# Optimization experiments

Measured on AMD Instinct MI355X. Metric: run time of the kernel, lower is better.

## Reference

```python
import jax, jax.numpy as jnp
import numpy as np

N = 100000          # nodes
E = 1600000         # edges (avg degree 16)
H = 128             # hidden_dim
P = 10              # INVARIANT_PHYSICS_DIM
TOTAL = P + H
LN_EPS = 1e-5       # torch LayerNorm default


def setup_inputs() -> dict:
    key = jax.random.key(0)
    ks = jax.random.split(key, 16)
    s = 0.02
    return {
        "physics_x": jax.random.normal(ks[0], (N, P), dtype=jnp.float32),
        "learnable_emb": jax.random.normal(ks[1], (N, H), dtype=jnp.float32),
        "edge_index": jax.random.randint(ks[2], (2, E), 0, N, dtype=jnp.int32),
        "Wq": jax.random.normal(ks[3], (TOTAL, H), dtype=jnp.float32) * s,
        "bq": jnp.zeros((H,), dtype=jnp.float32),
        "Wk": jax.random.normal(ks[4], (TOTAL, H), dtype=jnp.float32) * s,
        "bk": jnp.zeros((H,), dtype=jnp.float32),
        "Wv": jax.random.normal(ks[5], (H, H), dtype=jnp.float32) * s,
        "bv": jnp.zeros((H,), dtype=jnp.float32),
        "Wo": jax.random.normal(ks[6], (H, H), dtype=jnp.float32) * s,
        "bo": jnp.zeros((H,), dtype=jnp.float32),
        "gamma": jnp.ones((H,), dtype=jnp.float32),
        "beta": jnp.zeros((H,), dtype=jnp.float32),
    }


def reference(physics_x, learnable_emb, edge_index, Wq, bq, Wk, bk, Wv, bv, Wo, bo, gamma, beta):
    n_nodes = learnable_emb.shape[0]
    scale = 1.0 / np.sqrt(Wq.shape[1]).astype(np.float32)

    full_repr = jnp.concatenate([physics_x, learnable_emb], axis=-1)   # [N, P+H]
    Q = full_repr @ Wq + bq                                            # [N, H]
    K = full_repr @ Wk + bk                                            # [N, H]
    V = learnable_emb @ Wv + bv                                        # [N, H]

    src, dst = edge_index[0], edge_index[1]
    # per-edge unnormalized attention (NOTE: no max-subtraction, faithful to source)
    attn_scores = jnp.sum(Q[dst] * K[src], axis=-1) * scale            # [E]
    exp_scores = jnp.exp(attn_scores)                                  # [E]
    denom = jax.ops.segment_sum(exp_scores, dst, num_segments=n_nodes) # [N]
    attn_probs = exp_scores / (denom[dst] + 1e-8)                      # [E]

    msg = V[src] * attn_probs[:, None]                                 # [E, H]
    agg = jax.ops.segment_sum(msg, dst, num_segments=n_nodes)          # [N, H]

    out = agg @ Wo + bo
    x = learnable_emb + out
    mu = jnp.mean(x, axis=-1, keepdims=True)
    var = jnp.var(x, axis=-1, keepdims=True)
    return gamma * (x - mu) / jnp.sqrt(var + LN_EPS) + beta
```

## Files before the change

kernel.cpp:

```cpp
#include <hip/hip_runtime.h>
#include <hip/hip_bf16.h>
#include <math.h>

#define PDIM 10
#define HDIM 128
#define TDIM 138
#define AROW 168
#define B_LEN (5 * 8 * 64 * 8)
#define TROW 136

#define CW_WQ 0
#define CW_WK 17664
#define CW_WV 35328
#define CW_WO 51712
#define CW_BQ 68096
#define CW_BK 68224
#define CW_BV 68352
#define CW_BO 68480
#define CW_GA 68608
#define CW_BE 68736
#define CW_TOTAL 68864

typedef short v8s __attribute__((ext_vector_type(8)));
typedef float v4f __attribute__((ext_vector_type(4)));
typedef float v2f __attribute__((ext_vector_type(2)));

#if defined(__has_builtin)
#if __has_builtin(__builtin_amdgcn_cvt_pk_f32_fp8) && __has_builtin(__builtin_amdgcn_cvt_pk_fp8_f32)
#define HAVE_FP8_CVT 1
#endif
#endif
#ifndef HAVE_FP8_CVT
#define HAVE_FP8_CVT 0
#endif

__device__ __forceinline__ float b2f_lo(unsigned u) { return __uint_as_float(u << 16); }
__device__ __forceinline__ float b2f_hi(unsigned u) { return __uint_as_float(u & 0xffff0000u); }
__device__ __forceinline__ unsigned short f2b(float f) {
    unsigned u = __float_as_uint(f);
    u += 0x7fffu + ((u >> 16) & 1u);
    return (unsigned short)(u >> 16);
}

__device__ __forceinline__ float f8_dec1(unsigned b) {
    unsigned e = (b >> 3) & 0xf, m = b & 7;
    float v = e ? __uint_as_float(((e + 120) << 23) | (m << 20))
                : (float)m * 0.001953125f;
    return (b & 0x80) ? -v : v;
}
__device__ __forceinline__ unsigned f8_enc1(float f) {
    unsigned u = __float_as_uint(f);
    unsigned s = (u >> 31) << 7;
    float a = fabsf(f);
    if (a < 0.0009765625f) return s;
    if (a < 0.015625f) {
        int m = (int)(a * 512.f + 0.5f); if (m > 7) m = 7;
        return s | (unsigned)m;
    }
    if (a >= 448.f) return s | 0x7e;
    int ex = (int)((u >> 23) & 0xff);
    unsigned mant = u & 0x7fffff;
    unsigned r = mant >> 20, rem = mant & 0xfffff;
    if (rem > 0x80000u || (rem == 0x80000u && (r & 1))) r++;
    if (r == 8) { r = 0; ex++; }
    if (ex - 127 > 8) return s | 0x7e;
    return s | (unsigned)((ex - 120) << 3) | r;
}

__device__ __forceinline__ void dot4(unsigned w, const float* q, float& p) {
#if HAVE_FP8_CVT
    v2f lo = __builtin_amdgcn_cvt_pk_f32_fp8((int)w, false);
    v2f hi = __builtin_amdgcn_cvt_pk_f32_fp8((int)w, true);
    p = fmaf(q[0], lo[0], p); p = fmaf(q[1], lo[1], p);
    p = fmaf(q[2], hi[0], p); p = fmaf(q[3], hi[1], p);
#else
    p = fmaf(q[0], f8_dec1(w & 0xff), p);
    p = fmaf(q[1], f8_dec1((w >> 8) & 0xff), p);
    p = fmaf(q[2], f8_dec1((w >> 16) & 0xff), p);
    p = fmaf(q[3], f8_dec1(w >> 24), p);
#endif
}
__device__ __forceinline__ void acc4(unsigned w, float e, float* acc) {
#if HAVE_FP8_CVT
    v2f lo = __builtin_amdgcn_cvt_pk_f32_fp8((int)w, false);
    v2f hi = __builtin_amdgcn_cvt_pk_f32_fp8((int)w, true);
    acc[0] = fmaf(e, lo[0], acc[0]); acc[1] = fmaf(e, lo[1], acc[1]);
    acc[2] = fmaf(e, hi[0], acc[2]); acc[3] = fmaf(e, hi[1], acc[3]);
#else
    acc[0] = fmaf(e, f8_dec1(w & 0xff), acc[0]);
    acc[1] = fmaf(e, f8_dec1((w >> 8) & 0xff), acc[1]);
    acc[2] = fmaf(e, f8_dec1((w >> 16) & 0xff), acc[2]);
    acc[3] = fmaf(e, f8_dec1(w >> 24), acc[3]);
#endif
}
__device__ __forceinline__ uint2 pack8(uint4 t) {
#if HAVE_FP8_CVT
    int u0 = __builtin_amdgcn_cvt_pk_fp8_f32(b2f_lo(t.x), b2f_hi(t.x), 0, false);
    u0 = __builtin_amdgcn_cvt_pk_fp8_f32(b2f_lo(t.y), b2f_hi(t.y), u0, true);
    int u1 = __builtin_amdgcn_cvt_pk_fp8_f32(b2f_lo(t.z), b2f_hi(t.z), 0, false);
    u1 = __builtin_amdgcn_cvt_pk_fp8_f32(b2f_lo(t.w), b2f_hi(t.w), u1, true);
    return make_uint2((unsigned)u0, (unsigned)u1);
#else
    unsigned u0 = f8_enc1(b2f_lo(t.x)) | (f8_enc1(b2f_hi(t.x)) << 8)
                | (f8_enc1(b2f_lo(t.y)) << 16) | (f8_enc1(b2f_hi(t.y)) << 24);
    unsigned u1 = f8_enc1(b2f_lo(t.z)) | (f8_enc1(b2f_hi(t.z)) << 8)
                | (f8_enc1(b2f_lo(t.w)) << 16) | (f8_enc1(b2f_hi(t.w)) << 24);
    return make_uint2(u0, u1);
#endif
}

__global__ void ws_sentinel_kernel(float* out, int bucket)
{
    if (threadIdx.x == 0) out[0] = ldexpf(1.f + (float)bucket / 256.f, 100);
}

__global__ __launch_bounds__(256) void convert_weights(
    const float* Wq, const float* Wk, const float* Wv, const float* Wo,
    const float* bq, const float* bk, const float* bv, const float* bo,
    const float* ga, const float* be,
    float* __restrict__ dst)
{
    int idx = blockIdx.x * 256 + threadIdx.x;
    if (idx >= CW_TOTAL) return;
    const float* src; int loc;
    if      (idx < CW_WK) { src = Wq; loc = idx - CW_WQ; }
    else if (idx < CW_WV) { src = Wk; loc = idx - CW_WK; }
    else if (idx < CW_WO) { src = Wv; loc = idx - CW_WV; }
    else if (idx < CW_BQ) { src = Wo; loc = idx - CW_WO; }
    else if (idx < CW_BK) { src = bq; loc = idx - CW_BQ; }
    else if (idx < CW_BV) { src = bk; loc = idx - CW_BK; }
    else if (idx < CW_BO) { src = bv; loc = idx - CW_BV; }
    else if (idx < CW_GA) { src = bo; loc = idx - CW_BO; }
    else if (idx < CW_BE) { src = ga; loc = idx - CW_GA; }
    else                  { src = be; loc = idx - CW_BE; }
    dst[idx] = src[loc];
}

__global__ __launch_bounds__(256) void pack_wfrag(
    const float* __restrict__ cw, unsigned short* __restrict__ wfrag)
{
    int g = blockIdx.x * 256 + threadIdx.x;
    if (g >= 3 * 5 * 8 * 64) return;
    int lane = g & 63;
    int nt   = (g >> 6) & 7;
    int mk   = g >> 9;
    int kc = mk % 5, mat = mk / 5;
    int quad = lane >> 4, l15 = lane & 15;
    int n = nt * 16 + l15;

    unsigned short* dst = wfrag + (size_t)g * 8;
    #pragma unroll
    for (int j = 0; j < 8; ++j) {
        int k = kc * 32 + quad * 8 + j;
        float v = 0.f;
        if (mat == 0)      { if (k < TDIM) v = cw[CW_WQ + k * HDIM + n]; }
        else if (mat == 1) { if (k < TDIM) v = cw[CW_WK + k * HDIM + n]; }
        else               { if (k >= PDIM && k < TDIM) v = cw[CW_WV + (k - PDIM) * HDIM + n]; }
        dst[j] = f2b(v);
    }
}

__global__ __launch_bounds__(256, 5) void qkv_mfma_kernel(
    const float* __restrict__ physics, const float* __restrict__ emb,
    const float* __restrict__ cw, const unsigned short* __restrict__ wfrag,
    unsigned short* __restrict__ Qb, unsigned char* __restrict__ K8,
    unsigned char* __restrict__ V8, int n_nodes)
{
    __shared__ __align__(16) unsigned short smem[64 * AROW];

    const int tid = threadIdx.x;
    const int nbase = blockIdx.x * 64;
    const int lane = tid & 63;
    const int w = tid >> 6;
    const int quad = lane >> 4;
    const int l15 = lane & 15;

    for (int idx = tid; idx < 64 * 5; idx += 256) {
        int r = idx / 5, p = idx - r * 5;
        int node = nbase + r;
        float v0 = 0.f, v1 = 0.f;
        if (node < n_nodes) {
            const float* ph = physics + (size_t)node * PDIM + 2 * p;
            v0 = ph[0]; v1 = ph[1];
        }
        ((unsigned*)smem)[r * 84 + p] = (unsigned)f2b(v0) | ((unsigned)f2b(v1) << 16);
    }
    for (int idx = tid; idx < 64 * 32; idx += 256) {
        int r = idx >> 5, c = idx & 31;
        int node = nbase + r;
        float4 e = make_float4(0.f, 0.f, 0.f, 0.f);
        if (node < n_nodes) e = *(const float4*)(emb + (size_t)node * HDIM + 4 * c);
        unsigned* dst = (unsigned*)smem + r * 84 + 5 + 2 * c;
        dst[0] = (unsigned)f2b(e.x) | ((unsigned)f2b(e.y) << 16);
        dst[1] = (unsigned)f2b(e.z) | ((unsigned)f2b(e.w) << 16);
    }
    for (int idx = tid; idx < 64 * 15; idx += 256) {
        int r = idx / 15, p = idx - r * 15;
        ((unsigned*)smem)[r * 84 + 69 + p] = 0;
    }
    __syncthreads();

    v8s a_frag[5];
    #pragma unroll
    for (int kc = 0; kc < 5; ++kc)
        a_frag[kc] = *(v8s*)(smem + (w * 16 + l15) * AROW + kc * 32 + quad * 8);
    __syncthreads();

    const int r_out = tid >> 2;
    const int cseg = (tid & 3) * 32;
    const int node_out = nbase + r_out;

    for (int mat = 0; mat < 3; ++mat) {
        const v8s* bglob = (const v8s*)(wfrag + (size_t)mat * B_LEN) + lane;

        v4f acc[8];
        #pragma unroll
        for (int nt = 0; nt < 8; ++nt) acc[nt] = (v4f){0.f, 0.f, 0.f, 0.f};

        #pragma unroll
        for (int kc = 0; kc < 5; ++kc) {
            #pragma unroll
            for (int nt = 0; nt < 8; ++nt) {
                v8s b = bglob[(kc * 8 + nt) * 64];
                acc[nt] = __builtin_amdgcn_mfma_f32_16x16x32_bf16(
                    a_frag[kc], b, acc[nt], 0, 0, 0);
            }
        }

        #pragma unroll
        for (int nt = 0; nt < 8; ++nt) {
            float bias = cw[CW_BQ + mat * HDIM + nt * 16 + l15];
            #pragma unroll
            for (int reg = 0; reg < 4; ++reg) {
                int row = w * 16 + quad * 4 + reg;
                smem[row * TROW + nt * 16 + l15] = f2b(acc[nt][reg] + bias);
            }
        }
        __syncthreads();

        if (node_out < n_nodes) {
            const unsigned short* srcp = smem + r_out * TROW + cseg;
            if (mat == 0) {
                unsigned short* dst = Qb + (size_t)node_out * HDIM + cseg;
                #pragma unroll
                for (int j = 0; j < 4; ++j)
                    ((uint4*)dst)[j] = *(const uint4*)(srcp + 8 * j);
            } else {
                unsigned char* dst8 = (mat == 1 ? K8 : V8) + (size_t)node_out * HDIM + cseg;
                uint4 t0 = *(const uint4*)(srcp);
                uint4 t1 = *(const uint4*)(srcp + 8);
                uint4 t2 = *(const uint4*)(srcp + 16);
                uint4 t3 = *(const uint4*)(srcp + 24);
                uint2 p0 = pack8(t0), p1 = pack8(t1), p2 = pack8(t2), p3 = pack8(t3);
                ((uint4*)dst8)[0] = make_uint4(p0.x, p0.y, p1.x, p1.y);
                ((uint4*)dst8)[1] = make_uint4(p2.x, p2.y, p3.x, p3.y);
            }
        }
        if (mat < 2) __syncthreads();
    }
}

__global__ __launch_bounds__(256) void degree_kernel(
    const int* __restrict__ ei, int* __restrict__ deg, int n_edges, int n_nodes)
{
    int e = blockIdx.x * 256 + threadIdx.x;
    if (e < n_edges) {
        int d = ei[n_edges + e];
        d = max(0, min(d, n_nodes - 1));
        atomicAdd(&deg[d], 1);
    }
}

__global__ __launch_bounds__(256) void scan_bsum(
    const int* __restrict__ deg, int* __restrict__ bsum, int n)
{
    __shared__ int s[256];
    int i = blockIdx.x * 256 + threadIdx.x;
    s[threadIdx.x] = (i < n) ? deg[i] : 0;
    __syncthreads();
    for (int off = 128; off > 0; off >>= 1) {
        if (threadIdx.x < off) s[threadIdx.x] += s[threadIdx.x + off];
        __syncthreads();
    }
    if (threadIdx.x == 0) bsum[blockIdx.x] = s[0];
}

__global__ __launch_bounds__(512) void scan_boff(
    const int* __restrict__ bsum, int* __restrict__ boff, int nb)
{
    __shared__ int s[512];
    int t = threadIdx.x;
    int v = (t < nb) ? bsum[t] : 0;
    s[t] = v;
    __syncthreads();
    for (int off = 1; off < 512; off <<= 1) {
        int u = (t >= off) ? s[t - off] : 0;
        __syncthreads();
        s[t] += u;
        __syncthreads();
    }
    if (t < nb) boff[t] = s[t] - v;
}

__global__ __launch_bounds__(256) void scan_final(
    const int* __restrict__ deg, const int* __restrict__ boff,
    int* __restrict__ row_off, int n)
{
    __shared__ int s[256];
    int t = threadIdx.x;
    int i = blockIdx.x * 256 + t;
    int v = (i < n) ? deg[i] : 0;
    s[t] = v;
    __syncthreads();
    for (int off = 1; off < 256; off <<= 1) {
        int u = (t >= off) ? s[t - off] : 0;
        __syncthreads();
        s[t] += u;
        __syncthreads();
    }
    int base = boff[blockIdx.x];
    if (i < n) row_off[i] = base + s[t] - v;
    if (i == n - 1) row_off[n] = base + s[t];
}

__global__ __launch_bounds__(256) void fill_kernel(
    const int* __restrict__ ei, const int* __restrict__ row_off,
    int* __restrict__ cursor, int* __restrict__ csr_src, int n_edges, int n_nodes)
{
    int e = blockIdx.x * 256 + threadIdx.x;
    if (e < n_edges) {
        int d = ei[n_edges + e];
        d = max(0, min(d, n_nodes - 1));
        int pos = atomicAdd(&cursor[d], 1);
        csr_src[row_off[d] + pos] = ei[e];
    }
}

__global__ __launch_bounds__(256) void attn_fused_kernel(
    const unsigned short* __restrict__ Qb, const unsigned char* __restrict__ K8,
    const unsigned char* __restrict__ V8,
    const int* __restrict__ row_off, const int* __restrict__ csr_src,
    float* __restrict__ agg, int n_nodes, int n_edges)
{
    const int wid = (int)((blockIdx.x * 256 + threadIdx.x) >> 6);
    const int lane = threadIdx.x & 63;
    if (wid >= n_nodes) return;
    const int eg = lane >> 3;
    const int cg = lane & 7;

    const float scale = 0.088388347648318447f;
    const uint4* qp = (const uint4*)(Qb + (size_t)wid * HDIM + cg * 16);
    uint4 qa = qp[0], qb = qp[1];
    float q[16];
    q[0]  = b2f_lo(qa.x) * scale; q[1]  = b2f_hi(qa.x) * scale;
    q[2]  = b2f_lo(qa.y) * scale; q[3]  = b2f_hi(qa.y) * scale;
    q[4]  = b2f_lo(qa.z) * scale; q[5]  = b2f_hi(qa.z) * scale;
    q[6]  = b2f_lo(qa.w) * scale; q[7]  = b2f_hi(qa.w) * scale;
    q[8]  = b2f_lo(qb.x) * scale; q[9]  = b2f_hi(qb.x) * scale;
    q[10] = b2f_lo(qb.y) * scale; q[11] = b2f_hi(qb.y) * scale;
    q[12] = b2f_lo(qb.z) * scale; q[13] = b2f_hi(qb.z) * scale;
    q[14] = b2f_lo(qb.w) * scale; q[15] = b2f_hi(qb.w) * scale;

    int beg = row_off[wid], end = row_off[wid + 1];
    beg = max(0, min(beg, n_edges));
    end = max(beg, min(end, n_edges));

    float acc[16];
    #pragma unroll
    for (int j = 0; j < 16; ++j) acc[j] = 0.f;
    float den = 0.f;

    for (int i = beg; i < end; i += 8) {
        int idx = i + eg;
        bool valid = idx < end;
        int s = csr_src[valid ? idx : (end - 1)];
        s = max(0, min(s, n_nodes - 1));
        uint4 kr = *(const uint4*)(K8 + (size_t)s * HDIM + cg * 16);
        uint4 vr = *(const uint4*)(V8 + (size_t)s * HDIM + cg * 16);

        float p = 0.f;
        dot4(kr.x, q + 0, p);
        dot4(kr.y, q + 4, p);
        dot4(kr.z, q + 8, p);
        dot4(kr.w, q + 12, p);
        p += __shfl_xor(p, 1);
        p += __shfl_xor(p, 2);
        p += __shfl_xor(p, 4);

        float e = valid ? __expf(fminf(p, 60.f)) : 0.f;
        den += e;
        acc4(vr.x, e, acc + 0);
        acc4(vr.y, e, acc + 4);
        acc4(vr.z, e, acc + 8);
        acc4(vr.w, e, acc + 12);
    }

    #pragma unroll
    for (int j = 0; j < 16; ++j) {
        acc[j] += __shfl_xor(acc[j], 8);
        acc[j] += __shfl_xor(acc[j], 16);
        acc[j] += __shfl_xor(acc[j], 32);
    }
    den += __shfl_xor(den, 8);
    den += __shfl_xor(den, 16);
    den += __shfl_xor(den, 32);

    float inv = 1.f / (den + 1e-8f);
    if (eg == 0) {
        float* dst = agg + (size_t)wid * HDIM + cg * 16;
        #pragma unroll
        for (int j = 0; j < 4; ++j)
            *(float4*)(dst + 4 * j) = make_float4(acc[4*j] * inv, acc[4*j+1] * inv,
                                                 acc[4*j+2] * inv, acc[4*j+3] * inv);
    }
}

__global__ __launch_bounds__(256) void out_ln_kernel(
    const float* __restrict__ emb,
    const float* __restrict__ cw,
    float* __restrict__ out, int n_nodes)
{
    __shared__ float lds[HDIM * 32];
    const int tid = threadIdx.x;
    const int nbase = blockIdx.x * 32;

    for (int idx = tid; idx < 32 * HDIM; idx += 256) {
        int m = idx >> 7;
        int t = idx & 127;
        int node = nbase + m;
        lds[t * 32 + m] = (node < n_nodes) ? out[(size_t)node * HDIM + t] : 0.f;
    }
    __syncthreads();

    const int c = tid & 31;
    const int g = tid >> 5;
    const float* Wo = cw + CW_WO;

    float acc[4][4] = {{0.f}};
    for (int t = 0; t < HDIM; ++t) {
        float4 r = *(const float4*)(lds + t * 32 + 4 * g);
        float rr[4] = { r.x, r.y, r.z, r.w };
        float4 w4 = *(const float4*)(Wo + t * HDIM + 4 * c);
        float wa[4] = { w4.x, w4.y, w4.z, w4.w };
        #pragma unroll
        for (int m = 0; m < 4; ++m)
            #pragma unroll
            for (int j = 0; j < 4; ++j)
                acc[m][j] = fmaf(rr[m], wa[j], acc[m][j]);
    }

    float4 bo4 = *(const float4*)(cw + CW_BO + 4 * c);
    float4 ga4 = *(const float4*)(cw + CW_GA + 4 * c);
    float4 be4 = *(const float4*)(cw + CW_BE + 4 * c);
    float boa[4] = { bo4.x, bo4.y, bo4.z, bo4.w };
    float ga[4]  = { ga4.x, ga4.y, ga4.z, ga4.w };
    float ba[4]  = { be4.x, be4.y, be4.z, be4.w };

    #pragma unroll
    for (int m = 0; m < 4; ++m) {
        int node = nbase + 4 * g + m;
        float ea[4] = { 0.f, 0.f, 0.f, 0.f };
        if (node < n_nodes) {
            float4 e4 = *(const float4*)(emb + (size_t)node * HDIM + 4 * c);
            ea[0] = e4.x; ea[1] = e4.y; ea[2] = e4.z; ea[3] = e4.w;
        }

        float x[4], s1 = 0.f, s2 = 0.f;
        #pragma unroll
        for (int j = 0; j < 4; ++j) {
            x[j] = ea[j] + acc[m][j] + boa[j];
            s1 += x[j];
            s2 = fmaf(x[j], x[j], s2);
        }
        #pragma unroll
        for (int mask = 1; mask <= 16; mask <<= 1) {
            s1 += __shfl_xor(s1, mask);
            s2 += __shfl_xor(s2, mask);
        }
        float mu = s1 * (1.f / 128.f);
        float var = fmaxf(s2 * (1.f / 128.f) - mu * mu, 0.f);
        float rs = rsqrtf(var + 1e-5f);
        if (node < n_nodes) {
            float4 o;
            o.x = ga[0] * (x[0] - mu) * rs + ba[0];
            o.y = ga[1] * (x[1] - mu) * rs + ba[1];
            o.z = ga[2] * (x[2] - mu) * rs + ba[2];
            o.w = ga[3] * (x[3] - mu) * rs + ba[3];
            *(float4*)(out + (size_t)node * HDIM + 4 * c) = o;
        }
    }
}

extern "C" void kernel_launch(void* const* d_in, const int* in_sizes, int n_in,
                              void* d_out, int out_size, void* d_ws, size_t ws_size,
                              hipStream_t stream)
{
    const float* physics = (const float*)d_in[0];
    const float* emb     = (const float*)d_in[1];
    const int*   ei      = (const int*)d_in[2];

    const int n_nodes = in_sizes[1] / HDIM;
    const int n_edges = in_sizes[2] / 2;
    const int NB = (n_nodes + 255) / 256;

    char* ws = (char*)d_ws;
    size_t off = 0;
    auto alloc = [&](size_t bytes) -> void* {
        void* p = ws + off;
        off = (off + bytes + 255) & ~(size_t)255;
        return p;
    };

    float* cw      = (float*)alloc((size_t)CW_TOTAL * 4);
    unsigned short* wfrag = (unsigned short*)alloc((size_t)3 * B_LEN * 2);
    int* deg       = (int*)alloc((size_t)2 * n_nodes * 4);
    int* cursor    = deg + n_nodes;
    int* row_off   = (int*)alloc((size_t)(n_nodes + 1) * 4);
    int* bsum      = (int*)alloc((size_t)NB * 4);
    int* boff      = (int*)alloc((size_t)NB * 4);
    int* csr_src   = (int*)alloc((size_t)n_edges * 4);
    unsigned short* Qb = (unsigned short*)alloc((size_t)n_nodes * HDIM * 2);
    unsigned char* K8  = (unsigned char*)alloc((size_t)n_nodes * HDIM);
    unsigned char* V8  = (unsigned char*)alloc((size_t)n_nodes * HDIM);

    if (ws_size < off) {
        int bucket = (int)min((size_t)255, ws_size >> 24);
        ws_sentinel_kernel<<<1, 64, 0, stream>>>((float*)d_out, bucket);
        return;
    }

    hipMemsetAsync(deg, 0, (size_t)2 * n_nodes * sizeof(int), stream);

    convert_weights<<<(CW_TOTAL + 255) / 256, 256, 0, stream>>>(
        (const float*)d_in[3], (const float*)d_in[5], (const float*)d_in[7],
        (const float*)d_in[9], (const float*)d_in[4], (const float*)d_in[6],
        (const float*)d_in[8], (const float*)d_in[10], (const float*)d_in[11],
        (const float*)d_in[12], cw);

    pack_wfrag<<<(3 * 5 * 8 * 64 + 255) / 256, 256, 0, stream>>>(cw, wfrag);
    qkv_mfma_kernel<<<(n_nodes + 63) / 64, 256, 0, stream>>>(
        physics, emb, cw, wfrag, Qb, K8, V8, n_nodes);

    degree_kernel<<<(n_edges + 255) / 256, 256, 0, stream>>>(ei, deg, n_edges, n_nodes);
    scan_bsum<<<NB, 256, 0, stream>>>(deg, bsum, n_nodes);
    scan_boff<<<1, 512, 0, stream>>>(bsum, boff, NB);
    scan_final<<<NB, 256, 0, stream>>>(deg, boff, row_off, n_nodes);
    fill_kernel<<<(n_edges + 255) / 256, 256, 0, stream>>>(ei, row_off, cursor, csr_src, n_edges, n_nodes);

    attn_fused_kernel<<<(n_nodes + 3) / 4, 256, 0, stream>>>(
        Qb, K8, V8, row_off, csr_src, (float*)d_out, n_nodes, n_edges);

    out_ln_kernel<<<(n_nodes + 31) / 32, 256, 0, stream>>>(
        emb, cw, (float*)d_out, n_nodes);
}
```

Baseline: 469.4 us.

## Partition CSR fill by destination range and vectorize LN tile load

The CSR fill kernel now runs 8 destination-range partitions, and each block scans a chunk of edges while handling only the destinations in its partition. This is meant to keep the atomics on cursor and the scattered csr_src writes local to a smaller address range, improving L2 locality. The cost is reading the edge list eight times. Separately, out_ln_kernel loads its node tile with coalesced float4 reads into a padded row-major LDS layout instead of scalar transposed stores, and the inner loop now does four scalar LDS reads per step.

```diff
diff --git a/kernel.cpp b/kernel.cpp
--- a/kernel.cpp
+++ b/kernel.cpp
@@ -323,16 +323,28 @@
     if (i == n - 1) row_off[n] = base + s[t];
 }
 
-__global__ __launch_bounds__(256) void fill_kernel(
+#define FILL_NPART 8
+#define FILL_CHUNKS 512
+__global__ __launch_bounds__(256) void fill_part_kernel(
     const int* __restrict__ ei, const int* __restrict__ row_off,
     int* __restrict__ cursor, int* __restrict__ csr_src, int n_edges, int n_nodes)
 {
-    int e = blockIdx.x * 256 + threadIdx.x;
-    if (e < n_edges) {
+    const int part = blockIdx.x & (FILL_NPART - 1);
+    const int chunk = blockIdx.x >> 3;
+    const int W = (n_nodes + FILL_NPART - 1) / FILL_NPART;
+    const int lo = part * W;
+    const int hi = min(n_nodes, lo + W);
+    const int epc = (n_edges + FILL_CHUNKS - 1) / FILL_CHUNKS;
+    const int e0 = chunk * epc;
+    const int e1 = min(n_edges, e0 + epc);
+
+    for (int e = e0 + (int)threadIdx.x; e < e1; e += 256) {
         int d = ei[n_edges + e];
         d = max(0, min(d, n_nodes - 1));
-        int pos = atomicAdd(&cursor[d], 1);
-        csr_src[row_off[d] + pos] = ei[e];
+        if (d >= lo && d < hi) {
+            int pos = atomicAdd(&cursor[d], 1);
+            csr_src[row_off[d] + pos] = ei[e];
+        }
     }
 }
 
@@ -415,20 +427,23 @@
     }
 }
 
+#define LNROW 132
 __global__ __launch_bounds__(256) void out_ln_kernel(
     const float* __restrict__ emb,
     const float* __restrict__ cw,
     float* __restrict__ out, int n_nodes)
 {
-    __shared__ float lds[HDIM * 32];
+    __shared__ float lds[32 * LNROW];
     const int tid = threadIdx.x;
     const int nbase = blockIdx.x * 32;
 
-    for (int idx = tid; idx < 32 * HDIM; idx += 256) {
-        int m = idx >> 7;
-        int t = idx & 127;
+    for (int idx = tid; idx < 32 * 32; idx += 256) {
+        int m = idx >> 5;
+        int cc = idx & 31;
         int node = nbase + m;
-        lds[t * 32 + m] = (node < n_nodes) ? out[(size_t)node * HDIM + t] : 0.f;
+        float4 v = make_float4(0.f, 0.f, 0.f, 0.f);
+        if (node < n_nodes) v = *(const float4*)(out + (size_t)node * HDIM + 4 * cc);
+        *(float4*)(lds + m * LNROW + 4 * cc) = v;
     }
     __syncthreads();
 
@@ -438,8 +453,9 @@
 
     float acc[4][4] = {{0.f}};
     for (int t = 0; t < HDIM; ++t) {
-        float4 r = *(const float4*)(lds + t * 32 + 4 * g);
-        float rr[4] = { r.x, r.y, r.z, r.w };
+        float rr[4];
+        #pragma unroll
+        for (int m = 0; m < 4; ++m) rr[m] = lds[(4 * g + m) * LNROW + t];
         float4 w4 = *(const float4*)(Wo + t * HDIM + 4 * c);
         float wa[4] = { w4.x, w4.y, w4.z, w4.w };
         #pragma unroll
@@ -545,7 +561,8 @@
     scan_bsum<<<NB, 256, 0, stream>>>(deg, bsum, n_nodes);
     scan_boff<<<1, 512, 0, stream>>>(bsum, boff, NB);
     scan_final<<<NB, 256, 0, stream>>>(deg, boff, row_off, n_nodes);
-    fill_kernel<<<(n_edges + 255) / 256, 256, 0, stream>>>(ei, row_off, cursor, csr_src, n_edges, n_nodes);
+    fill_part_kernel<<<FILL_NPART * FILL_CHUNKS, 256, 0, stream>>>(
+        ei, row_off, cursor, csr_src, n_edges, n_nodes);
 
     attn_fused_kernel<<<(n_nodes + 3) / 4, 256, 0, stream>>>(
         Qb, K8, V8, row_off, csr_src, (float*)d_out, n_nodes, n_edges);
```

Result: faster. 457.4 us (-2.6%).
